# Optimization experiments

Measured on AMD Instinct MI355X. Metric: run time of the kernel, lower is better.

## Reference

```python
import jax, jax.numpy as jnp
import numpy as np

D_MODEL = 512
D_STATE = 128
D_CONV = 4
EXPAND = 2
HEADDIM = 64
NGROUPS = 1
D_INNER = EXPAND * D_MODEL            # 1024
NHEADS = D_INNER // HEADDIM           # 16
CONV_DIM = D_INNER + 2 * NGROUPS * D_STATE   # 1280
D_IN_PROJ = 2 * D_INNER + 2 * NGROUPS * D_STATE + NHEADS  # 2320
EPS = 1e-5


def _silu(v):
    return v * jax.nn.sigmoid(v)


def setup_inputs() -> dict:
    key = jax.random.key(0)
    ks = jax.random.split(key, 8)
    B, L = 2, 1024
    x = jax.random.normal(ks[0], (B, L, D_MODEL), jnp.float32)
    in_proj_w = jax.random.normal(ks[1], (D_IN_PROJ, D_MODEL), jnp.float32) * (D_MODEL ** -0.5)
    conv_w = jax.random.normal(ks[2], (CONV_DIM, D_CONV), jnp.float32) * (D_CONV ** -0.5)
    conv_b = jnp.zeros((CONV_DIM,), jnp.float32)
    # dt_bias = softplus^-1(dt) for dt ~ U[1e-3, 0.1]  (Mamba2 init)
    dt = jax.random.uniform(ks[3], (NHEADS,), jnp.float32, 0.001, 0.1)
    dt_bias = jnp.log(jnp.expm1(dt))
    A_log = jnp.log(jax.random.uniform(ks[4], (NHEADS,), jnp.float32, 1.0, 16.0))
    D = jnp.ones((NHEADS,), jnp.float32)
    norm_w = jnp.ones((D_INNER,), jnp.float32)
    out_proj_w = jax.random.normal(ks[5], (D_MODEL, D_INNER), jnp.float32) * (D_INNER ** -0.5)
    return dict(x=x, in_proj_w=in_proj_w, conv_w=conv_w, conv_b=conv_b,
                dt_bias=dt_bias, A_log=A_log, D=D, norm_w=norm_w, out_proj_w=out_proj_w)


def _mamba2(x, in_proj_w, conv_w, conv_b, dt_bias, A_log, D, norm_w, out_proj_w):
    Bb, L, _ = x.shape
    # input projection -> [z | xBC | dt]
    zxbcdt = jnp.einsum('bld,ed->ble', x, in_proj_w)          # (B,L,2320)
    z = zxbcdt[..., :D_INNER]                                  # (B,L,1024)
    xBC = zxbcdt[..., D_INNER:D_INNER + CONV_DIM]              # (B,L,1280)
    dt = jax.nn.softplus(zxbcdt[..., D_INNER + CONV_DIM:] + dt_bias)  # (B,L,H)
    # causal depthwise conv1d over L + SiLU
    lhs = jnp.transpose(xBC, (0, 2, 1))                        # (B,C,L)
    rhs = conv_w[:, None, :]                                   # (C,1,K)
    conv = jax.lax.conv_general_dilated(
        lhs, rhs, window_strides=(1,), padding=[(D_CONV - 1, 0)],
        dimension_numbers=('NCH', 'OIH', 'NCH'), feature_group_count=CONV_DIM)
    xBC = _silu(jnp.transpose(conv, (0, 2, 1)) + conv_b)       # (B,L,1280)
    xs = xBC[..., :D_INNER].reshape(Bb, L, NHEADS, HEADDIM)    # (B,L,H,P)
    Bmat = xBC[..., D_INNER:D_INNER + D_STATE]                 # (B,L,N) ngroups=1
    Cmat = xBC[..., D_INNER + D_STATE:]                        # (B,L,N)
    # selective scan: h_t = exp(dt_t*A)*h_{t-1} + (dt_t*x_t) outer B_t ; y_t = C_t . h_t
    A = -jnp.exp(A_log)                                        # (H,)
    dA = jnp.exp(dt * A)                                       # (B,L,H)
    dx = dt[..., None] * xs                                    # (B,L,H,P)

    def step(h, inp):
        dA_t, dx_t, B_t, C_t = inp                             # (B,H),(B,H,P),(B,N),(B,N)
        h = h * dA_t[..., None, None] + dx_t[..., None] * B_t[:, None, None, :]
        y = jnp.einsum('bhpn,bn->bhp', h, C_t)
        return h, y

    h0 = jnp.zeros((Bb, NHEADS, HEADDIM, D_STATE), x.dtype)
    _, ys = jax.lax.scan(step, h0, (jnp.moveaxis(dA, 1, 0), jnp.moveaxis(dx, 1, 0),
                                    jnp.moveaxis(Bmat, 1, 0), jnp.moveaxis(Cmat, 1, 0)))
    y = jnp.moveaxis(ys, 0, 1) + xs * D[None, None, :, None]   # (B,L,H,P)
    y = y.reshape(Bb, L, D_INNER)
    # gated RMSNorm: rmsnorm(y * silu(z)) * w
    g = y * _silu(z)
    g = g * jax.lax.rsqrt(jnp.mean(g * g, axis=-1, keepdims=True) + EPS) * norm_w
    return jnp.einsum('ble,de->bld', g, out_proj_w)            # (B,L,d_model)


def reference(x, in_proj_w, conv_w, conv_b, dt_bias, A_log, D, norm_w, out_proj_w):
    return _mamba2(x, in_proj_w, conv_w, conv_b, dt_bias, A_log, D, norm_w, out_proj_w)
```

## Files before the change

kernel.cpp:

```cpp
#include <hip/hip_runtime.h>
#include <math.h>

#define BATCH 2
#define SEQ 1024
#define DM 512
#define DI 1024
#define DS 128
#define NH 16
#define HD 64
#define CONVD 1280
#define DPROJ 2320
#define ROWS (BATCH*SEQ)
#define NCH 16
#define CHK 64
#define NPAD 2432

typedef unsigned short u16;
typedef unsigned int   u32;
typedef u16   u16x4 __attribute__((ext_vector_type(4)));
typedef u16   u16x8 __attribute__((ext_vector_type(8)));
typedef short bf16x8 __attribute__((ext_vector_type(8)));
typedef float f32x4 __attribute__((ext_vector_type(4)));

__device__ __forceinline__ u16 f2bf(float f) {
    u32 u = __float_as_uint(f);
    return (u16)((u + 0x7fffu + ((u >> 16) & 1u)) >> 16);
}
__device__ __forceinline__ float bf2f(u16 h) {
    return __uint_as_float(((u32)h) << 16);
}
__device__ __forceinline__ void gl_lds16(const u16* g, u16* lds) {
    __builtin_amdgcn_global_load_lds((const __attribute__((address_space(1))) void*)g,
                                     (__attribute__((address_space(3))) void*)lds,
                                     16, 0, 0);
}

__device__ __forceinline__ int swz_off(int row, int q, int SLROW) {
    return (row*SLROW + (q ^ (row & 7)))*8;
}
template<int SLROW>
__device__ __forceinline__ void stage64(const u16* gbase, int gstride, u16* lds, int tid) {
    #pragma unroll
    for (int j = 0; j < (64*SLROW)/256; ++j) {
        int slot = j*256 + tid;
        int row = slot / SLROW;
        int pos = slot % SLROW;
        gl_lds16(gbase + (size_t)row*gstride + (pos ^ (row & 7))*8, lds + slot*8);
    }
}

__device__ __forceinline__ void cvt_blk(const float* __restrict__ src,
                                        u16* __restrict__ dst,
                                        int blk, int n_src, int n_total) {
    int idx = (blk*256 + threadIdx.x)*8;
    if (idx >= n_total) return;
    u16x8 o;
    if (idx + 8 <= n_src) {
        float4 a = *reinterpret_cast<const float4*>(src + idx);
        float4 b = *reinterpret_cast<const float4*>(src + idx + 4);
        o[0]=f2bf(a.x); o[1]=f2bf(a.y); o[2]=f2bf(a.z); o[3]=f2bf(a.w);
        o[4]=f2bf(b.x); o[5]=f2bf(b.y); o[6]=f2bf(b.z); o[7]=f2bf(b.w);
    } else {
        #pragma unroll
        for (int e = 0; e < 8; ++e)
            o[e] = (idx + e < n_src) ? f2bf(src[idx + e]) : (u16)0;
    }
    *reinterpret_cast<u16x8*>(dst + idx) = o;
}

__global__ __launch_bounds__(256) void k_prep(const float* __restrict__ x,
                                              const float* __restrict__ W,
                                              const float* __restrict__ Wo,
                                              const float* __restrict__ dt_bias,
                                              const float* __restrict__ A_log,
                                              u16* __restrict__ xb,
                                              u16* __restrict__ Wb,
                                              u16* __restrict__ Wob,
                                              float* __restrict__ dtb,
                                              float* __restrict__ abuf) {
    int bid = blockIdx.x;
    if (bid < 512) { cvt_blk(x, xb, bid, ROWS*DM, ROWS*DM); return; }
    if (bid < 1120) { cvt_blk(W, Wb, bid-512, DPROJ*DM, NPAD*DM); return; }
    if (bid < 1376) { cvt_blk(Wo, Wob, bid-1120, DM*DI, DM*DI); return; }
    int wave = threadIdx.x >> 6, lane = threadIdx.x & 63;
    int row = (bid-1376)*4 + wave;
    int h = lane & 15, part = lane >> 4;
    const float* xr = x + (size_t)row * DM + part*128;
    const float* wr = W + (size_t)(DI + CONVD + h) * DM + part*128;
    float acc = 0.f;
    #pragma unroll 4
    for (int j = 0; j < 32; ++j) {
        float4 xv = *reinterpret_cast<const float4*>(xr + j*4);
        float4 wv = *reinterpret_cast<const float4*>(wr + j*4);
        acc += xv.x*wv.x + xv.y*wv.y + xv.z*wv.z + xv.w*wv.w;
    }
    acc += __shfl_xor(acc, 16);
    acc += __shfl_xor(acc, 32);
    if (part == 0) {
        float v = acc + dt_bias[h];
        float dt = (v > 20.f) ? v : log1pf(expf(v));
        dtb[row*NH + h]  = dt;
        abuf[row*NH + h] = dt * (-expf(A_log[h]));
    }
}

template<int BM, int BN, int K, bool BF16OUT>
__global__ __launch_bounds__(256) void k_gemm(const u16* __restrict__ A,
                                              const u16* __restrict__ B,
                                              void* __restrict__ Cv,
                                              int ldc, int ncols) {
    constexpr int WTM = BM/2, WTN = BN/2, FM = WTM/16, FN = WTN/16;
    constexpr int CA = BM*4/256, CB = BN*4/256;
    __shared__ u16 As[BM*32];
    __shared__ u16 Bs[BN*32];
    int tid  = threadIdx.x;
    int lane = tid & 63, wave = tid >> 6;
    int wr = wave >> 1, wc = wave & 1;
    size_t bm = (size_t)blockIdx.y * BM, bn = (size_t)blockIdx.x * BN;

    const u16* srcA[CA]; u16* dstA[CA];
    #pragma unroll
    for (int j = 0; j < CA; ++j) {
        int i = j*256 + tid;
        int row = i >> 2, q = (i & 3) ^ ((row >> 1) & 3);
        srcA[j] = A + (bm + row) * (size_t)K + q*8;
        dstA[j] = As + i*8;
    }
    const u16* srcB[CB]; u16* dstB[CB];
    #pragma unroll
    for (int j = 0; j < CB; ++j) {
        int i = j*256 + tid;
        int row = i >> 2, q = (i & 3) ^ ((row >> 1) & 3);
        srcB[j] = B + (bn + row) * (size_t)K + q*8;
        dstB[j] = Bs + i*8;
    }

    int kq = lane >> 4;
    int aoff[FM], boff[FN];
    #pragma unroll
    for (int fi = 0; fi < FM; ++fi) {
        int row = wr*WTM + fi*16 + (lane & 15);
        aoff[fi] = (row*4 + (kq ^ ((row >> 1) & 3))) * 8;
    }
    #pragma unroll
    for (int fj = 0; fj < FN; ++fj) {
        int row = wc*WTN + fj*16 + (lane & 15);
        boff[fj] = (row*4 + (kq ^ ((row >> 1) & 3))) * 8;
    }

    f32x4 acc[FM][FN];
    #pragma unroll
    for (int fi = 0; fi < FM; ++fi)
        #pragma unroll
        for (int fj = 0; fj < FN; ++fj)
            acc[fi][fj] = (f32x4){0.f, 0.f, 0.f, 0.f};

    for (int k0 = 0; k0 < K; k0 += 32) {
        __syncthreads();
        #pragma unroll
        for (int j = 0; j < CA; ++j) gl_lds16(srcA[j] + k0, dstA[j]);
        #pragma unroll
        for (int j = 0; j < CB; ++j) gl_lds16(srcB[j] + k0, dstB[j]);
        __syncthreads();
        bf16x8 av[FM], bv[FN];
        #pragma unroll
        for (int fi = 0; fi < FM; ++fi)
            av[fi] = *reinterpret_cast<const bf16x8*>(As + aoff[fi]);
        #pragma unroll
        for (int fj = 0; fj < FN; ++fj)
            bv[fj] = *reinterpret_cast<const bf16x8*>(Bs + boff[fj]);
        #pragma unroll
        for (int fi = 0; fi < FM; ++fi)
            #pragma unroll
            for (int fj = 0; fj < FN; ++fj)
                acc[fi][fj] = __builtin_amdgcn_mfma_f32_16x16x32_bf16(
                    av[fi], bv[fj], acc[fi][fj], 0, 0, 0);
    }

    #pragma unroll
    for (int fi = 0; fi < FM; ++fi) {
        size_t grow0 = bm + wr*WTM + fi*16 + (lane >> 4)*4;
        #pragma unroll
        for (int fj = 0; fj < FN; ++fj) {
            size_t gcol = bn + wc*WTN + fj*16 + (lane & 15);
            if ((int)gcol < ncols) {
                #pragma unroll
                for (int r = 0; r < 4; ++r) {
                    if constexpr (BF16OUT)
                        ((u16*)Cv)[(grow0 + r)*ldc + gcol] = f2bf(acc[fi][fj][r]);
                    else
                        ((float*)Cv)[(grow0 + r)*ldc + gcol] = acc[fi][fj][r];
                }
            }
        }
    }
}

__global__ __launch_bounds__(320) void k_conv(const u16* __restrict__ zx,
                                              const float* __restrict__ cw,
                                              const float* __restrict__ cb,
                                              u16* __restrict__ convo) {
    int row = blockIdx.x;
    int l   = row & (SEQ-1);
    int c0  = threadIdx.x * 4;

    const float4* cw4 = reinterpret_cast<const float4*>(cw);
    float4 w0 = cw4[c0+0], w1 = cw4[c0+1], w2 = cw4[c0+2], w3 = cw4[c0+3];
    const float* wa0 = &w0.x; const float* wa1 = &w1.x;
    const float* wa2 = &w2.x; const float* wa3 = &w3.x;

    float4 bv = *reinterpret_cast<const float4*>(cb + c0);
    float acc0 = bv.x, acc1 = bv.y, acc2 = bv.z, acc3 = bv.w;

    #pragma unroll
    for (int k = 0; k < 4; ++k) {
        int lk = l - 3 + k;
        if (lk < 0) continue;
        u16x4 v = *reinterpret_cast<const u16x4*>(zx + (size_t)(row-3+k)*DPROJ + DI + c0);
        acc0 += bf2f(v[0]) * wa0[k];
        acc1 += bf2f(v[1]) * wa1[k];
        acc2 += bf2f(v[2]) * wa2[k];
        acc3 += bf2f(v[3]) * wa3[k];
    }
    u16x4 o;
    o[0] = f2bf(acc0 / (1.f + expf(-acc0)));
    o[1] = f2bf(acc1 / (1.f + expf(-acc1)));
    o[2] = f2bf(acc2 / (1.f + expf(-acc2)));
    o[3] = f2bf(acc3 / (1.f + expf(-acc3)));
    *reinterpret_cast<u16x4*>(convo + (size_t)row*CONVD + c0) = o;
}

__global__ __launch_bounds__(256) void k_chunk_state(
    const u16* __restrict__ convo, const float* __restrict__ dtb,
    const float* __restrict__ abuf, u16* __restrict__ Sb,
    float* __restrict__ Pbuf) {
    int blk = blockIdx.x;
    int c  = blk & (NCH-1);
    int h  = (blk >> 4) & (NH-1);
    int b  = blk >> 8;
    int row0 = b*SEQ + c*CHK;
    int tid = threadIdx.x, lane = tid & 63, wave = tid >> 6;
    int wr = wave >> 1, wc = wave & 1;

    __shared__ u16 xsT[64*64];
    __shared__ u16 BT[128*64];
    __shared__ float s_coef[CHK];

    int st = tid >> 2, q = tid & 3;
    const u16* r = convo + (size_t)(row0 + st)*CONVD;
    u16x8 xa = *reinterpret_cast<const u16x8*>(r + h*HD + q*16);
    u16x8 xc = *reinterpret_cast<const u16x8*>(r + h*HD + q*16 + 8);
    u16x8 b0 = *reinterpret_cast<const u16x8*>(r + DI + q*32);
    u16x8 b1 = *reinterpret_cast<const u16x8*>(r + DI + q*32 + 8);
    u16x8 b2 = *reinterpret_cast<const u16x8*>(r + DI + q*32 + 16);
    u16x8 b3 = *reinterpret_cast<const u16x8*>(r + DI + q*32 + 24);

    if (tid < CHK) {
        float v = abuf[(size_t)(row0 + tid)*NH + h];
        #pragma unroll
        for (int off = 1; off < 64; off <<= 1) {
            float o = __shfl_up(v, off);
            if (tid >= off) v += o;
        }
        float vend = __shfl(v, 63);
        float dt = dtb[(size_t)(row0 + tid)*NH + h];
        s_coef[tid] = dt * expf(vend - v);
        if (tid == 63) Pbuf[blk] = expf(vend);
    }
    __syncthreads();

    float cf = s_coef[st];
    #pragma unroll
    for (int e = 0; e < 16; ++e) {
        int p = q*16 + e;
        u16 xv = (e < 8) ? xa[e] : xc[e-8];
        xsT[(p*8 + ((st>>3) ^ (p&7)))*8 + (st&7)] = f2bf(cf * bf2f(xv));
    }
    #pragma unroll
    for (int e = 0; e < 32; ++e) {
        int n = q*32 + e;
        u16 bvv = (e < 8) ? b0[e] : (e < 16) ? b1[e-8] : (e < 24) ? b2[e-16] : b3[e-24];
        BT[(n*8 + ((st>>3) ^ (n&7)))*8 + (st&7)] = bvv;
    }
    __syncthreads();

    int kq = lane >> 4, fr = lane & 15;
    f32x4 acc[2][4];
    #pragma unroll
    for (int fi = 0; fi < 2; ++fi)
        #pragma unroll
        for (int fj = 0; fj < 4; ++fj)
            acc[fi][fj] = (f32x4){0.f,0.f,0.f,0.f};

    #pragma unroll
    for (int ks = 0; ks < 2; ++ks) {
        bf16x8 av[2], bv[4];
        #pragma unroll
        for (int fi = 0; fi < 2; ++fi)
            av[fi] = *reinterpret_cast<const bf16x8*>(xsT + swz_off(wr*32 + fi*16 + fr, ks*4 + kq, 8));
        #pragma unroll
        for (int fj = 0; fj < 4; ++fj)
            bv[fj] = *reinterpret_cast<const bf16x8*>(BT + swz_off(wc*64 + fj*16 + fr, ks*4 + kq, 8));
        #pragma unroll
        for (int fi = 0; fi < 2; ++fi)
            #pragma unroll
            for (int fj = 0; fj < 4; ++fj)
                acc[fi][fj] = __builtin_amdgcn_mfma_f32_16x16x32_bf16(av[fi], bv[fj], acc[fi][fj], 0,0,0);
    }

    u16* outp = Sb + (size_t)blk*(HD*DS);
    #pragma unroll
    for (int fi = 0; fi < 2; ++fi)
        #pragma unroll
        for (int rr = 0; rr < 4; ++rr) {
            int p = wr*32 + fi*16 + kq*4 + rr;
            #pragma unroll
            for (int fj = 0; fj < 4; ++fj) {
                int n = wc*64 + fj*16 + fr;
                outp[(size_t)p*DS + n] = f2bf(acc[fi][fj][rr]);
            }
        }
}

__global__ __launch_bounds__(256) void k_state_pass(u16* __restrict__ Sb,
                                                    const float* __restrict__ Pbuf) {
    int bh = blockIdx.x;
    int off = threadIdx.x * 32;
    float hr[32];
    #pragma unroll
    for (int j = 0; j < 32; ++j) hr[j] = 0.f;

    for (int c = 0; c < NCH; ++c) {
        u16* base = Sb + ((size_t)(bh*NCH + c))*(HD*DS) + off;
        float P = Pbuf[bh*NCH + c];
        float s[32];
        #pragma unroll
        for (int j = 0; j < 4; ++j) {
            u16x8 v = *reinterpret_cast<const u16x8*>(base + j*8);
            #pragma unroll
            for (int e = 0; e < 8; ++e) s[j*8+e] = bf2f(v[e]);
        }
        #pragma unroll
        for (int j = 0; j < 4; ++j) {
            u16x8 w;
            #pragma unroll
            for (int e = 0; e < 8; ++e) w[e] = f2bf(hr[j*8+e]);
            *reinterpret_cast<u16x8*>(base + j*8) = w;
        }
        #pragma unroll
        for (int j = 0; j < 32; ++j) hr[j] = hr[j]*P + s[j];
    }
}

__global__ __launch_bounds__(256) void k_chunk_out(
    const u16* __restrict__ convo, const float* __restrict__ dtb,
    const float* __restrict__ abuf, const u16* __restrict__ Sb,
    const float* __restrict__ Dp, u16* __restrict__ ybuf) {
    int blk = blockIdx.x;
    int c  = blk & (NCH-1);
    int h  = (blk >> 4) & (NH-1);
    int b  = blk >> 8;
    int row0 = b*SEQ + c*CHK;
    int tid = threadIdx.x, lane = tid & 63, wave = tid >> 6;
    int wr = wave >> 1, wc = wave & 1;

    __shared__ u16 Ct[64*128];
    __shared__ u16 Bh[64*128];
    __shared__ u16 Mt[64*64];
    __shared__ u16 dxT[64*64];
    __shared__ float s_cum[CHK];
    __shared__ float s_dt[CHK];

    const u16* cbase = convo + (size_t)row0*CONVD;

    stage64<16>(cbase + DI + DS, CONVD, Ct, tid);
    stage64<16>(cbase + DI,      CONVD, Bh, tid);

    int st = tid >> 2, q = tid & 3;
    u16x8 xr0 = *reinterpret_cast<const u16x8*>(cbase + (size_t)st*CONVD + h*HD + q*16);
    u16x8 xr1 = *reinterpret_cast<const u16x8*>(cbase + (size_t)st*CONVD + h*HD + q*16 + 8);

    if (tid < CHK) {
        float v = abuf[(size_t)(row0 + tid)*NH + h];
        #pragma unroll
        for (int off = 1; off < 64; off <<= 1) {
            float o = __shfl_up(v, off);
            if (tid >= off) v += o;
        }
        s_cum[tid] = v;
        s_dt[tid] = dtb[(size_t)(row0 + tid)*NH + h];
    }
    __syncthreads();

    #pragma unroll
    for (int e = 0; e < 16; ++e) {
        int p = q*16 + e;
        u16 xv = (e < 8) ? xr0[e] : xr1[e-8];
        dxT[(p*8 + ((st>>3) ^ (p&7)))*8 + (st&7)] = xv;
    }

    int kq = lane >> 4, fr = lane & 15;

    f32x4 macc[2][2];
    #pragma unroll
    for (int fi = 0; fi < 2; ++fi)
        #pragma unroll
        for (int fj = 0; fj < 2; ++fj)
            macc[fi][fj] = (f32x4){0.f,0.f,0.f,0.f};
    #pragma unroll
    for (int ks = 0; ks < 4; ++ks) {
        bf16x8 av[2], bv[2];
        #pragma unroll
        for (int fi = 0; fi < 2; ++fi)
            av[fi] = *reinterpret_cast<const bf16x8*>(Ct + swz_off(wr*32 + fi*16 + fr, ks*4 + kq, 16));
        #pragma unroll
        for (int fj = 0; fj < 2; ++fj)
            bv[fj] = *reinterpret_cast<const bf16x8*>(Bh + swz_off(wc*32 + fj*16 + fr, ks*4 + kq, 16));
        #pragma unroll
        for (int fi = 0; fi < 2; ++fi)
            #pragma unroll
            for (int fj = 0; fj < 2; ++fj)
                macc[fi][fj] = __builtin_amdgcn_mfma_f32_16x16x32_bf16(av[fi], bv[fj], macc[fi][fj], 0,0,0);
    }

    #pragma unroll
    for (int fi = 0; fi < 2; ++fi)
        #pragma unroll
        for (int rr = 0; rr < 4; ++rr) {
            int t = wr*32 + fi*16 + kq*4 + rr;
            float cumt = s_cum[t];
            #pragma unroll
            for (int fj = 0; fj < 2; ++fj) {
                int s = wc*32 + fj*16 + fr;
                float val = (s <= t) ? macc[fi][fj][rr] * expf(cumt - s_cum[s]) * s_dt[s] : 0.f;
                Mt[(t*8 + ((s>>3) ^ (t&7)))*8 + (s&7)] = f2bf(val);
            }
        }
    __syncthreads();

    stage64<16>(Sb + (size_t)blk*(HD*DS), DS, Bh, tid);

    f32x4 accY[2][2];
    #pragma unroll
    for (int fi = 0; fi < 2; ++fi)
        #pragma unroll
        for (int fj = 0; fj < 2; ++fj)
            accY[fi][fj] = (f32x4){0.f,0.f,0.f,0.f};
    #pragma unroll
    for (int ks = 0; ks < 2; ++ks) {
        bf16x8 av[2], bv[2];
        #pragma unroll
        for (int fi = 0; fi < 2; ++fi)
            av[fi] = *reinterpret_cast<const bf16x8*>(Mt + swz_off(wr*32 + fi*16 + fr, ks*4 + kq, 8));
        #pragma unroll
        for (int fj = 0; fj < 2; ++fj)
            bv[fj] = *reinterpret_cast<const bf16x8*>(dxT + swz_off(wc*32 + fj*16 + fr, ks*4 + kq, 8));
        #pragma unroll
        for (int fi = 0; fi < 2; ++fi)
            #pragma unroll
            for (int fj = 0; fj < 2; ++fj)
                accY[fi][fj] = __builtin_amdgcn_mfma_f32_16x16x32_bf16(av[fi], bv[fj], accY[fi][fj], 0,0,0);
    }
    __syncthreads();

    f32x4 accD[2][2];
    #pragma unroll
    for (int fi = 0; fi < 2; ++fi)
        #pragma unroll
        for (int fj = 0; fj < 2; ++fj)
            accD[fi][fj] = (f32x4){0.f,0.f,0.f,0.f};
    #pragma unroll
    for (int ks = 0; ks < 4; ++ks) {
        bf16x8 av[2], bv[2];
        #pragma unroll
        for (int fi = 0; fi < 2; ++fi)
            av[fi] = *reinterpret_cast<const bf16x8*>(Ct + swz_off(wr*32 + fi*16 + fr, ks*4 + kq, 16));
        #pragma unroll
        for (int fj = 0; fj < 2; ++fj)
            bv[fj] = *reinterpret_cast<const bf16x8*>(Bh + swz_off(wc*32 + fj*16 + fr, ks*4 + kq, 16));
        #pragma unroll
        for (int fi = 0; fi < 2; ++fi)
            #pragma unroll
            for (int fj = 0; fj < 2; ++fj)
                accD[fi][fj] = __builtin_amdgcn_mfma_f32_16x16x32_bf16(av[fi], bv[fj], accD[fi][fj], 0,0,0);
    }

    float Dv = Dp[h];
    #pragma unroll
    for (int fi = 0; fi < 2; ++fi)
        #pragma unroll
        for (int rr = 0; rr < 4; ++rr) {
            int t = wr*32 + fi*16 + kq*4 + rr;
            float et = expf(s_cum[t]);
            #pragma unroll
            for (int fj = 0; fj < 2; ++fj) {
                int p = wc*32 + fj*16 + fr;
                float xs = bf2f(cbase[(size_t)t*CONVD + h*HD + p]);
                float y = accY[fi][fj][rr] + et*accD[fi][fj][rr] + Dv*xs;
                ybuf[(size_t)(row0 + t)*DI + h*HD + p] = f2bf(y);
            }
        }
}

__global__ __launch_bounds__(256) void k_gate(const u16* __restrict__ zx,
                                              const u16* __restrict__ ybuf,
                                              const float* __restrict__ nw,
                                              u16* __restrict__ g) {
    int row = blockIdx.x;
    int t = threadIdx.x;
    const u16* zr = zx + (size_t)row*DPROJ;
    const u16* yr = ybuf + (size_t)row*DI;

    u16x4 zv = *reinterpret_cast<const u16x4*>(zr + t*4);
    u16x4 yv = *reinterpret_cast<const u16x4*>(yr + t*4);
    float gv[4];
    float ss = 0.f;
    #pragma unroll
    for (int j = 0; j < 4; ++j) {
        float z = bf2f(zv[j]), y = bf2f(yv[j]);
        float sz = z / (1.f + expf(-z));
        float gg = y * sz;
        gv[j] = gg;
        ss += gg*gg;
    }
    ss += __shfl_xor(ss, 1);
    ss += __shfl_xor(ss, 2);
    ss += __shfl_xor(ss, 4);
    ss += __shfl_xor(ss, 8);
    ss += __shfl_xor(ss, 16);
    ss += __shfl_xor(ss, 32);
    __shared__ float ls[4];
    if ((t & 63) == 0) ls[t >> 6] = ss;
    __syncthreads();
    float tot = ls[0] + ls[1] + ls[2] + ls[3];
    float scale = rsqrtf(tot * (1.f/DI) + 1e-5f);

    float4 nv = *reinterpret_cast<const float4*>(nw + t*4);
    const float* na = &nv.x;
    u16x4 og = { f2bf(gv[0]*scale*na[0]), f2bf(gv[1]*scale*na[1]),
                 f2bf(gv[2]*scale*na[2]), f2bf(gv[3]*scale*na[3]) };
    *reinterpret_cast<u16x4*>(g + (size_t)row*DI + t*4) = og;
}

extern "C" void kernel_launch(void* const* d_in, const int* in_sizes, int n_in,
                              void* d_out, int out_size, void* d_ws, size_t ws_size,
                              hipStream_t stream) {
    const float* x         = (const float*)d_in[0];
    const float* in_proj_w = (const float*)d_in[1];
    const float* conv_w    = (const float*)d_in[2];
    const float* conv_b    = (const float*)d_in[3];
    const float* dt_bias   = (const float*)d_in[4];
    const float* A_log     = (const float*)d_in[5];
    const float* Dp        = (const float*)d_in[6];
    const float* norm_w    = (const float*)d_in[7];
    const float* out_proj_w= (const float*)d_in[8];
    float* out = (float*)d_out;

    char* p = (char*)d_ws;
    u16*   zxb   = (u16*)p;   p += (size_t)ROWS*DPROJ*2;
    u16*   convo = (u16*)p;   p += (size_t)ROWS*CONVD*2;
    float* dtb   = (float*)p; p += (size_t)ROWS*NH*4;
    float* abuf  = (float*)p; p += (size_t)ROWS*NH*4;
    u16*   ybuf  = (u16*)p;   p += (size_t)ROWS*DI*2;
    u16*   xb    = (u16*)p;   p += (size_t)ROWS*DM*2;
    u16*   Wb    = (u16*)p;   p += (size_t)NPAD*DM*2;
    u16*   Wob   = (u16*)p;   p += (size_t)DM*DI*2;
    u16*   Sb    = (u16*)p;   p += (size_t)BATCH*NH*NCH*HD*DS*2;
    float* Pbuf  = (float*)p; p += 512*4;
    u16*   gb    = (u16*)p;   p += (size_t)ROWS*DI*2;

    k_prep<<<1888, 256, 0, stream>>>(x, in_proj_w, out_proj_w, dt_bias, A_log,
                                     xb, Wb, Wob, dtb, abuf);

    k_gemm<64,128,512,true><<<dim3(NPAD/128, ROWS/64), 256, 0, stream>>>(xb, Wb, zxb, DPROJ, DPROJ);

    k_conv<<<ROWS, CONVD/4, 0, stream>>>(zxb, conv_w, conv_b, convo);

    k_chunk_state<<<BATCH*NH*NCH, 256, 0, stream>>>(convo, dtb, abuf, Sb, Pbuf);
    k_state_pass <<<BATCH*NH, 256, 0, stream>>>(Sb, Pbuf);
    k_chunk_out  <<<BATCH*NH*NCH, 256, 0, stream>>>(convo, dtb, abuf, Sb, Dp, ybuf);

    k_gate<<<ROWS, 256, 0, stream>>>(zxb, ybuf, norm_w, gb);

    k_gemm<64,64,1024,false><<<dim3(DM/64, ROWS/64), 256, 0, stream>>>(gb, Wob, out, DM, DM);
}
```

Before: 91.23 us.

## Fuse conv into chunk kernels, double-buffer GEMM, parallelize state pass

Drops the standalone conv kernel and its convo buffer. The causal depthwise conv plus SiLU is recomputed from zxb inside k_chunk_state and k_chunk_out, and the D-skip term is read from shared memory. The GEMM moves to a 64-wide K tile with double-buffered LDS prefetch, and the first projection uses 128x128 tiles. k_state_pass is split across 8 segments per head for more parallelism. This removes one launch and a round trip through global memory, at the cost of redundant conv arithmetic (B/C rows recomputed by every head block) and fewer GEMM blocks.

```diff
diff --git a/kernel.cpp b/kernel.cpp
--- a/kernel.cpp
+++ b/kernel.cpp
@@ -46,6 +46,41 @@
         int row = slot / SLROW;
         int pos = slot % SLROW;
         gl_lds16(gbase + (size_t)row*gstride + (pos ^ (row & 7))*8, lds + slot*8);
+    }
+}
+
+__device__ __forceinline__ void conv16(const u16* __restrict__ zxb, int b, int c, int st,
+                                       int col0, const float* __restrict__ cw,
+                                       const float* __restrict__ cb,
+                                       float* __restrict__ acc) {
+    u16x8 w0[4], w1[4];
+    #pragma unroll
+    for (int k = 0; k < 4; ++k) {
+        int l = c*CHK + st - 3 + k;
+        if (l >= 0) {
+            const u16* r = zxb + ((size_t)b*SEQ + l)*DPROJ + DI + col0;
+            w0[k] = *reinterpret_cast<const u16x8*>(r);
+            w1[k] = *reinterpret_cast<const u16x8*>(r + 8);
+        } else {
+            w0[k] = (u16x8){0,0,0,0,0,0,0,0};
+            w1[k] = (u16x8){0,0,0,0,0,0,0,0};
+        }
+    }
+    float4 bias[4];
+    #pragma unroll
+    for (int j = 0; j < 4; ++j)
+        bias[j] = *reinterpret_cast<const float4*>(cb + col0 + j*4);
+    const float* ba = &bias[0].x;
+    #pragma unroll
+    for (int e = 0; e < 16; ++e) {
+        float4 w = *reinterpret_cast<const float4*>(cw + (size_t)(col0+e)*4);
+        float v = ba[e];
+        float x0 = bf2f(e<8 ? w0[0][e] : w1[0][e-8]);
+        float x1 = bf2f(e<8 ? w0[1][e] : w1[1][e-8]);
+        float x2 = bf2f(e<8 ? w0[2][e] : w1[2][e-8]);
+        float x3 = bf2f(e<8 ? w0[3][e] : w1[3][e-8]);
+        v += x0*w.x + x1*w.y + x2*w.z + x3*w.w;
+        acc[e] = v / (1.f + expf(-v));
     }
 }
 
@@ -109,80 +144,93 @@
                                               const u16* __restrict__ B,
                                               void* __restrict__ Cv,
                                               int ldc, int ncols) {
+    constexpr int BK = 64;
+    constexpr int NK = K / BK;
     constexpr int WTM = BM/2, WTN = BN/2, FM = WTM/16, FN = WTN/16;
-    constexpr int CA = BM*4/256, CB = BN*4/256;
-    __shared__ u16 As[BM*32];
-    __shared__ u16 Bs[BN*32];
-    int tid  = threadIdx.x;
-    int lane = tid & 63, wave = tid >> 6;
+    constexpr int CA = BM/32, CB = BN/32;
+    constexpr int TA = BM*8, TB = BN*8;
+    __shared__ u16 As[2*TA*8];
+    __shared__ u16 Bs[2*TB*8];
+    int tid = threadIdx.x, lane = tid & 63, wave = tid >> 6;
     int wr = wave >> 1, wc = wave & 1;
     size_t bm = (size_t)blockIdx.y * BM, bn = (size_t)blockIdx.x * BN;
 
-    const u16* srcA[CA]; u16* dstA[CA];
+    const u16* sA[CA]; int dA[CA];
     #pragma unroll
     for (int j = 0; j < CA; ++j) {
-        int i = j*256 + tid;
-        int row = i >> 2, q = (i & 3) ^ ((row >> 1) & 3);
-        srcA[j] = A + (bm + row) * (size_t)K + q*8;
-        dstA[j] = As + i*8;
-    }
-    const u16* srcB[CB]; u16* dstB[CB];
+        int i = j*256 + tid, row = i >> 3, pos = i & 7;
+        sA[j] = A + (bm + row)*(size_t)K + (pos ^ (row & 7))*8;
+        dA[j] = i*8;
+    }
+    const u16* sB[CB]; int dB[CB];
     #pragma unroll
     for (int j = 0; j < CB; ++j) {
-        int i = j*256 + tid;
-        int row = i >> 2, q = (i & 3) ^ ((row >> 1) & 3);
-        srcB[j] = B + (bn + row) * (size_t)K + q*8;
-        dstB[j] = Bs + i*8;
-    }
-
-    int kq = lane >> 4;
-    int aoff[FM], boff[FN];
+        int i = j*256 + tid, row = i >> 3, pos = i & 7;
+        sB[j] = B + (bn + row)*(size_t)K + (pos ^ (row & 7))*8;
+        dB[j] = i*8;
+    }
+
+    int fr = lane & 15, kq = lane >> 4;
+    int ar[FM], br[FN];
+    #pragma unroll
+    for (int fi = 0; fi < FM; ++fi) ar[fi] = wr*WTM + fi*16 + fr;
+    #pragma unroll
+    for (int fj = 0; fj < FN; ++fj) br[fj] = wc*WTN + fj*16 + fr;
+
+    f32x4 acc[FM][FN];
+    #pragma unroll
+    for (int fi = 0; fi < FM; ++fi)
+        #pragma unroll
+        for (int fj = 0; fj < FN; ++fj)
+            acc[fi][fj] = (f32x4){0.f,0.f,0.f,0.f};
+
+    #pragma unroll
+    for (int j = 0; j < CA; ++j) gl_lds16(sA[j], As + dA[j]);
+    #pragma unroll
+    for (int j = 0; j < CB; ++j) gl_lds16(sB[j], Bs + dB[j]);
+    asm volatile("s_waitcnt vmcnt(0)" ::: "memory");
+    __builtin_amdgcn_s_barrier();
+
+    int cur = 0;
+    #pragma unroll 1
+    for (int step = 0; step < NK; ++step) {
+        if (step + 1 < NK) {
+            int k0 = (step+1)*BK;
+            int nb = cur ^ 1;
+            #pragma unroll
+            for (int j = 0; j < CA; ++j) gl_lds16(sA[j] + k0, As + nb*TA*8 + dA[j]);
+            #pragma unroll
+            for (int j = 0; j < CB; ++j) gl_lds16(sB[j] + k0, Bs + nb*TB*8 + dB[j]);
+        }
+        const u16* Ab = As + cur*TA*8;
+        const u16* Bb = Bs + cur*TB*8;
+        #pragma unroll
+        for (int ks = 0; ks < 2; ++ks) {
+            bf16x8 av[FM], bv[FN];
+            #pragma unroll
+            for (int fi = 0; fi < FM; ++fi)
+                av[fi] = *reinterpret_cast<const bf16x8*>(Ab + (ar[fi]*8 + ((ks*4+kq) ^ (ar[fi]&7)))*8);
+            #pragma unroll
+            for (int fj = 0; fj < FN; ++fj)
+                bv[fj] = *reinterpret_cast<const bf16x8*>(Bb + (br[fj]*8 + ((ks*4+kq) ^ (br[fj]&7)))*8);
+            #pragma unroll
+            for (int fi = 0; fi < FM; ++fi)
+                #pragma unroll
+                for (int fj = 0; fj < FN; ++fj)
+                    acc[fi][fj] = __builtin_amdgcn_mfma_f32_16x16x32_bf16(
+                        av[fi], bv[fj], acc[fi][fj], 0, 0, 0);
+        }
+        asm volatile("s_waitcnt vmcnt(0)" ::: "memory");
+        __builtin_amdgcn_s_barrier();
+        cur ^= 1;
+    }
+
     #pragma unroll
     for (int fi = 0; fi < FM; ++fi) {
-        int row = wr*WTM + fi*16 + (lane & 15);
-        aoff[fi] = (row*4 + (kq ^ ((row >> 1) & 3))) * 8;
-    }
-    #pragma unroll
-    for (int fj = 0; fj < FN; ++fj) {
-        int row = wc*WTN + fj*16 + (lane & 15);
-        boff[fj] = (row*4 + (kq ^ ((row >> 1) & 3))) * 8;
-    }
-
-    f32x4 acc[FM][FN];
-    #pragma unroll
-    for (int fi = 0; fi < FM; ++fi)
-        #pragma unroll
-        for (int fj = 0; fj < FN; ++fj)
-            acc[fi][fj] = (f32x4){0.f, 0.f, 0.f, 0.f};
-
-    for (int k0 = 0; k0 < K; k0 += 32) {
-        __syncthreads();
-        #pragma unroll
-        for (int j = 0; j < CA; ++j) gl_lds16(srcA[j] + k0, dstA[j]);
-        #pragma unroll
-        for (int j = 0; j < CB; ++j) gl_lds16(srcB[j] + k0, dstB[j]);
-        __syncthreads();
-        bf16x8 av[FM], bv[FN];
-        #pragma unroll
-        for (int fi = 0; fi < FM; ++fi)
-            av[fi] = *reinterpret_cast<const bf16x8*>(As + aoff[fi]);
-        #pragma unroll
-        for (int fj = 0; fj < FN; ++fj)
-            bv[fj] = *reinterpret_cast<const bf16x8*>(Bs + boff[fj]);
-        #pragma unroll
-        for (int fi = 0; fi < FM; ++fi)
-            #pragma unroll
-            for (int fj = 0; fj < FN; ++fj)
-                acc[fi][fj] = __builtin_amdgcn_mfma_f32_16x16x32_bf16(
-                    av[fi], bv[fj], acc[fi][fj], 0, 0, 0);
-    }
-
-    #pragma unroll
-    for (int fi = 0; fi < FM; ++fi) {
-        size_t grow0 = bm + wr*WTM + fi*16 + (lane >> 4)*4;
+        size_t grow0 = bm + wr*WTM + fi*16 + kq*4;
         #pragma unroll
         for (int fj = 0; fj < FN; ++fj) {
-            size_t gcol = bn + wc*WTN + fj*16 + (lane & 15);
+            size_t gcol = bn + wc*WTN + fj*16 + fr;
             if ((int)gcol < ncols) {
                 #pragma unroll
                 for (int r = 0; r < 4; ++r) {
@@ -196,42 +244,9 @@
     }
 }
 
-__global__ __launch_bounds__(320) void k_conv(const u16* __restrict__ zx,
-                                              const float* __restrict__ cw,
-                                              const float* __restrict__ cb,
-                                              u16* __restrict__ convo) {
-    int row = blockIdx.x;
-    int l   = row & (SEQ-1);
-    int c0  = threadIdx.x * 4;
-
-    const float4* cw4 = reinterpret_cast<const float4*>(cw);
-    float4 w0 = cw4[c0+0], w1 = cw4[c0+1], w2 = cw4[c0+2], w3 = cw4[c0+3];
-    const float* wa0 = &w0.x; const float* wa1 = &w1.x;
-    const float* wa2 = &w2.x; const float* wa3 = &w3.x;
-
-    float4 bv = *reinterpret_cast<const float4*>(cb + c0);
-    float acc0 = bv.x, acc1 = bv.y, acc2 = bv.z, acc3 = bv.w;
-
-    #pragma unroll
-    for (int k = 0; k < 4; ++k) {
-        int lk = l - 3 + k;
-        if (lk < 0) continue;
-        u16x4 v = *reinterpret_cast<const u16x4*>(zx + (size_t)(row-3+k)*DPROJ + DI + c0);
-        acc0 += bf2f(v[0]) * wa0[k];
-        acc1 += bf2f(v[1]) * wa1[k];
-        acc2 += bf2f(v[2]) * wa2[k];
-        acc3 += bf2f(v[3]) * wa3[k];
-    }
-    u16x4 o;
-    o[0] = f2bf(acc0 / (1.f + expf(-acc0)));
-    o[1] = f2bf(acc1 / (1.f + expf(-acc1)));
-    o[2] = f2bf(acc2 / (1.f + expf(-acc2)));
-    o[3] = f2bf(acc3 / (1.f + expf(-acc3)));
-    *reinterpret_cast<u16x4*>(convo + (size_t)row*CONVD + c0) = o;
-}
-
 __global__ __launch_bounds__(256) void k_chunk_state(
-    const u16* __restrict__ convo, const float* __restrict__ dtb,
+    const u16* __restrict__ zxb, const float* __restrict__ cw,
+    const float* __restrict__ cb, const float* __restrict__ dtb,
     const float* __restrict__ abuf, u16* __restrict__ Sb,
     float* __restrict__ Pbuf) {
     int blk = blockIdx.x;
@@ -247,13 +262,6 @@
     __shared__ float s_coef[CHK];
 
     int st = tid >> 2, q = tid & 3;
-    const u16* r = convo + (size_t)(row0 + st)*CONVD;
-    u16x8 xa = *reinterpret_cast<const u16x8*>(r + h*HD + q*16);
-    u16x8 xc = *reinterpret_cast<const u16x8*>(r + h*HD + q*16 + 8);
-    u16x8 b0 = *reinterpret_cast<const u16x8*>(r + DI + q*32);
-    u16x8 b1 = *reinterpret_cast<const u16x8*>(r + DI + q*32 + 8);
-    u16x8 b2 = *reinterpret_cast<const u16x8*>(r + DI + q*32 + 16);
-    u16x8 b3 = *reinterpret_cast<const u16x8*>(r + DI + q*32 + 24);
 
     if (tid < CHK) {
         float v = abuf[(size_t)(row0 + tid)*NH + h];
@@ -267,20 +275,26 @@
         s_coef[tid] = dt * expf(vend - v);
         if (tid == 63) Pbuf[blk] = expf(vend);
     }
+
+    #pragma unroll
+    for (int g = 0; g < 2; ++g) {
+        float acc[16];
+        conv16(zxb, b, c, st, DI + q*32 + g*16, cw, cb, acc);
+        #pragma unroll
+        for (int e = 0; e < 16; ++e) {
+            int n = q*32 + g*16 + e;
+            BT[(n*8 + ((st>>3) ^ (n&7)))*8 + (st&7)] = f2bf(acc[e]);
+        }
+    }
+    float xsa[16];
+    conv16(zxb, b, c, st, h*HD + q*16, cw, cb, xsa);
     __syncthreads();
 
     float cf = s_coef[st];
     #pragma unroll
     for (int e = 0; e < 16; ++e) {
         int p = q*16 + e;
-        u16 xv = (e < 8) ? xa[e] : xc[e-8];
-        xsT[(p*8 + ((st>>3) ^ (p&7)))*8 + (st&7)] = f2bf(cf * bf2f(xv));
-    }
-    #pragma unroll
-    for (int e = 0; e < 32; ++e) {
-        int n = q*32 + e;
-        u16 bvv = (e < 8) ? b0[e] : (e < 16) ? b1[e-8] : (e < 24) ? b2[e-16] : b3[e-24];
-        BT[(n*8 + ((st>>3) ^ (n&7)))*8 + (st&7)] = bvv;
+        xsT[(p*8 + ((st>>3) ^ (p&7)))*8 + (st&7)] = f2bf(cf * xsa[e]);
     }
     __syncthreads();
 
@@ -324,36 +338,26 @@
 
 __global__ __launch_bounds__(256) void k_state_pass(u16* __restrict__ Sb,
                                                     const float* __restrict__ Pbuf) {
-    int bh = blockIdx.x;
-    int off = threadIdx.x * 32;
-    float hr[32];
-    #pragma unroll
-    for (int j = 0; j < 32; ++j) hr[j] = 0.f;
-
-    for (int c = 0; c < NCH; ++c) {
-        u16* base = Sb + ((size_t)(bh*NCH + c))*(HD*DS) + off;
-        float P = Pbuf[bh*NCH + c];
-        float s[32];
-        #pragma unroll
-        for (int j = 0; j < 4; ++j) {
-            u16x8 v = *reinterpret_cast<const u16x8*>(base + j*8);
-            #pragma unroll
-            for (int e = 0; e < 8; ++e) s[j*8+e] = bf2f(v[e]);
-        }
-        #pragma unroll
-        for (int j = 0; j < 4; ++j) {
-            u16x8 w;
-            #pragma unroll
-            for (int e = 0; e < 8; ++e) w[e] = f2bf(hr[j*8+e]);
-            *reinterpret_cast<u16x8*>(base + j*8) = w;
-        }
-        #pragma unroll
-        for (int j = 0; j < 32; ++j) hr[j] = hr[j]*P + s[j];
+    int bh = blockIdx.x >> 3, seg = blockIdx.x & 7;
+    int off = seg*1024 + threadIdx.x*4;
+    u16x4 s[NCH];
+    #pragma unroll
+    for (int cc = 0; cc < NCH; ++cc)
+        s[cc] = *reinterpret_cast<const u16x4*>(Sb + ((size_t)(bh*NCH + cc))*(HD*DS) + off);
+    float hr[4] = {0.f,0.f,0.f,0.f};
+    #pragma unroll
+    for (int cc = 0; cc < NCH; ++cc) {
+        u16x4 w = { f2bf(hr[0]), f2bf(hr[1]), f2bf(hr[2]), f2bf(hr[3]) };
+        *reinterpret_cast<u16x4*>(Sb + ((size_t)(bh*NCH + cc))*(HD*DS) + off) = w;
+        float P = Pbuf[bh*NCH + cc];
+        #pragma unroll
+        for (int j = 0; j < 4; ++j) hr[j] = hr[j]*P + bf2f(s[cc][j]);
     }
 }
 
 __global__ __launch_bounds__(256) void k_chunk_out(
-    const u16* __restrict__ convo, const float* __restrict__ dtb,
+    const u16* __restrict__ zxb, const float* __restrict__ cw,
+    const float* __restrict__ cb, const float* __restrict__ dtb,
     const float* __restrict__ abuf, const u16* __restrict__ Sb,
     const float* __restrict__ Dp, u16* __restrict__ ybuf) {
     int blk = blockIdx.x;
@@ -371,14 +375,7 @@
     __shared__ float s_cum[CHK];
     __shared__ float s_dt[CHK];
 
-    const u16* cbase = convo + (size_t)row0*CONVD;
-
-    stage64<16>(cbase + DI + DS, CONVD, Ct, tid);
-    stage64<16>(cbase + DI,      CONVD, Bh, tid);
-
     int st = tid >> 2, q = tid & 3;
-    u16x8 xr0 = *reinterpret_cast<const u16x8*>(cbase + (size_t)st*CONVD + h*HD + q*16);
-    u16x8 xr1 = *reinterpret_cast<const u16x8*>(cbase + (size_t)st*CONVD + h*HD + q*16 + 8);
 
     if (tid < CHK) {
         float v = abuf[(size_t)(row0 + tid)*NH + h];
@@ -390,14 +387,43 @@
         s_cum[tid] = v;
         s_dt[tid] = dtb[(size_t)(row0 + tid)*NH + h];
     }
+
+    #pragma unroll
+    for (int g = 0; g < 2; ++g) {
+        float acc[16];
+        conv16(zxb, b, c, st, DI + DS + q*32 + g*16, cw, cb, acc);
+        int slot0 = q*4 + g*2;
+        #pragma unroll
+        for (int hh = 0; hh < 2; ++hh) {
+            u16x8 o;
+            #pragma unroll
+            for (int e = 0; e < 8; ++e) o[e] = f2bf(acc[hh*8 + e]);
+            *reinterpret_cast<u16x8*>(Ct + (st*16 + ((slot0+hh) ^ (st&7)))*8) = o;
+        }
+    }
+    #pragma unroll
+    for (int g = 0; g < 2; ++g) {
+        float acc[16];
+        conv16(zxb, b, c, st, DI + q*32 + g*16, cw, cb, acc);
+        int slot0 = q*4 + g*2;
+        #pragma unroll
+        for (int hh = 0; hh < 2; ++hh) {
+            u16x8 o;
+            #pragma unroll
+            for (int e = 0; e < 8; ++e) o[e] = f2bf(acc[hh*8 + e]);
+            *reinterpret_cast<u16x8*>(Bh + (st*16 + ((slot0+hh) ^ (st&7)))*8) = o;
+        }
+    }
+    {
+        float acc[16];
+        conv16(zxb, b, c, st, h*HD + q*16, cw, cb, acc);
+        #pragma unroll
+        for (int e = 0; e < 16; ++e) {
+            int p = q*16 + e;
+            dxT[(p*8 + ((st>>3) ^ (p&7)))*8 + (st&7)] = f2bf(acc[e]);
+        }
+    }
     __syncthreads();
-
-    #pragma unroll
-    for (int e = 0; e < 16; ++e) {
-        int p = q*16 + e;
-        u16 xv = (e < 8) ? xr0[e] : xr1[e-8];
-        dxT[(p*8 + ((st>>3) ^ (p&7)))*8 + (st&7)] = xv;
-    }
 
     int kq = lane >> 4, fr = lane & 15;
 
@@ -495,7 +521,7 @@
             #pragma unroll
             for (int fj = 0; fj < 2; ++fj) {
                 int p = wc*32 + fj*16 + fr;
-                float xs = bf2f(cbase[(size_t)t*CONVD + h*HD + p]);
+                float xs = bf2f(dxT[(p*8 + ((t>>3) ^ (p&7)))*8 + (t&7)]);
                 float y = accY[fi][fj][rr] + et*accD[fi][fj][rr] + Dv*xs;
                 ybuf[(size_t)(row0 + t)*DI + h*HD + p] = f2bf(y);
             }
@@ -558,7 +584,6 @@
 
     char* p = (char*)d_ws;
     u16*   zxb   = (u16*)p;   p += (size_t)ROWS*DPROJ*2;
-    u16*   convo = (u16*)p;   p += (size_t)ROWS*CONVD*2;
     float* dtb   = (float*)p; p += (size_t)ROWS*NH*4;
     float* abuf  = (float*)p; p += (size_t)ROWS*NH*4;
     u16*   ybuf  = (u16*)p;   p += (size_t)ROWS*DI*2;
@@ -572,13 +597,11 @@
     k_prep<<<1888, 256, 0, stream>>>(x, in_proj_w, out_proj_w, dt_bias, A_log,
                                      xb, Wb, Wob, dtb, abuf);
 
-    k_gemm<64,128,512,true><<<dim3(NPAD/128, ROWS/64), 256, 0, stream>>>(xb, Wb, zxb, DPROJ, DPROJ);
-
-    k_conv<<<ROWS, CONVD/4, 0, stream>>>(zxb, conv_w, conv_b, convo);
-
-    k_chunk_state<<<BATCH*NH*NCH, 256, 0, stream>>>(convo, dtb, abuf, Sb, Pbuf);
-    k_state_pass <<<BATCH*NH, 256, 0, stream>>>(Sb, Pbuf);
-    k_chunk_out  <<<BATCH*NH*NCH, 256, 0, stream>>>(convo, dtb, abuf, Sb, Dp, ybuf);
+    k_gemm<128,128,512,true><<<dim3(NPAD/128, ROWS/128), 256, 0, stream>>>(xb, Wb, zxb, DPROJ, DPROJ);
+
+    k_chunk_state<<<BATCH*NH*NCH, 256, 0, stream>>>(zxb, conv_w, conv_b, dtb, abuf, Sb, Pbuf);
+    k_state_pass <<<BATCH*NH*8, 256, 0, stream>>>(Sb, Pbuf);
+    k_chunk_out  <<<BATCH*NH*NCH, 256, 0, stream>>>(zxb, conv_w, conv_b, dtb, abuf, Sb, Dp, ybuf);
 
     k_gate<<<ROWS, 256, 0, stream>>>(zxb, ybuf, norm_w, gb);
 
```

Measured after the change: 103.5 us. 13.5% more time.
